# Kernel optimization log

Hardware: AMD Instinct MI355X
Metric: run time of the kernel (lower is better)

The kernel has to match this reference:

```python
import jax, jax.numpy as jnp
import numpy as np

B, N, C, H = 2, 1024, 768, 12
D = C // H
SCALE = D ** -0.5


def setup_inputs() -> dict:
    key = jax.random.key(0)
    ks = jax.random.split(key, 6)
    s = 1.0 / np.sqrt(C)
    return {
        "x": jax.random.normal(ks[0], (B, N, C), jnp.float32),
        "Wqkv": jax.random.normal(ks[1], (3 * C, C), jnp.float32) * s,   # qkv_bias=False
        "Wa": jax.random.normal(ks[2], (H, C), jnp.float32) * s,        # selective gate Linear(dim, H)
        "ba": jnp.zeros((H,), jnp.float32),
        "Wproj": jax.random.normal(ks[3], (C, C), jnp.float32) * s,
        "bproj": jnp.zeros((C,), jnp.float32),
    }


def _silu_shifted(z):
    # silu(x) + 0.5, L2-normalized over head dim (silunorm=True)
    r = jax.nn.silu(z) + 0.5
    return r / jnp.linalg.norm(r, axis=-1, keepdims=True)


def _forward(x, Wqkv, Wa, ba, Wproj, bproj):
    qkv = (x @ Wqkv.T).reshape(B, N, 3, H, D).transpose(2, 0, 3, 1, 4)  # [3,B,H,N,D]
    q = _silu_shifted(qkv[0])
    k = _silu_shifted(qkv[1])
    v = qkv[2]

    # selective forget gates: a = 1 - sigmoid(Linear(x)); torch.tensor(...) detaches -> stop_gradient
    a = jax.lax.stop_gradient(1.0 - jax.nn.sigmoid(x @ Wa.T + ba)).transpose(0, 2, 1)  # [B,H,N]
    # drop first token's gate, prepend 1 (as in the module)
    a = jnp.concatenate([jnp.ones_like(a[..., :1]), a[..., 1:]], axis=-1)

    # Causal_Mask_Selective(log(a)):
    #   A_for[i,j]  = prod_{t=j..i-1} a[t]   (j <= i)
    #   A_back[i,j] = prod_{t=i+1..j} a[t]   (j >= i)
    #   M = A_for + A_back - I
    c = jnp.cumsum(jnp.log(a), axis=-1)
    c = jnp.concatenate([jnp.zeros_like(c[..., :1]), c], axis=-1)  # [B,H,N+1], c[m] = sum log a[0..m-1]
    tri = jnp.tril(jnp.ones((N, N), bool))
    d_for = c[..., :N, None] - c[..., None, :N]      # c[i]-c[j]
    d_back = c[..., None, 1:] - c[..., 1:, None]     # c[j+1]-c[i+1]
    A_for = jnp.where(tri, jnp.exp(jnp.where(tri, d_for, 0.0)), 0.0)
    A_back = jnp.where(tri.T, jnp.exp(jnp.where(tri.T, d_back, 0.0)), 0.0)
    M = A_for + A_back - jnp.eye(N, dtype=x.dtype)

    attn = jnp.einsum('bhid,bhjd->bhij', q, k) * SCALE * M
    attn = attn / (attn.sum(axis=-1, keepdims=True) + 1e-6)  # sum-normalization, NOT softmax
    out = jnp.einsum('bhij,bhjd->bhid', attn, v).transpose(0, 2, 1, 3).reshape(B, N, C)
    return out @ Wproj.T + bproj


def reference(x, Wqkv, Wa, ba, Wproj, bproj):
    return _forward(x, Wqkv, Wa, ba, Wproj, bproj)
```

## Files before the change

kernel.cpp:

```cpp
#include <hip/hip_runtime.h>
#include <hip/hip_bf16.h>

#define BB 2
#define NN 1024
#define CC 768
#define HH 12
#define DD 64
#define SCALE_F 0.125f

typedef __attribute__((ext_vector_type(8))) __bf16 bf16x8;
typedef __attribute__((ext_vector_type(8))) unsigned short u16x8;
typedef __attribute__((ext_vector_type(4))) unsigned short u16x4;
typedef __attribute__((ext_vector_type(4))) float f32x4;

static __device__ __forceinline__ bf16x8 as_bf16x8(u16x8 v) {
  return __builtin_bit_cast(bf16x8, v);
}
static __device__ __forceinline__ unsigned short bf16u(float f) {
  __hip_bfloat16 h = __float2bfloat16(f);
  return __builtin_bit_cast(unsigned short, h);
}
static __device__ __forceinline__ void gload16(const void* g, void* l) {
  __builtin_amdgcn_global_load_lds(
      (const __attribute__((address_space(1))) unsigned int*)g,
      (__attribute__((address_space(3))) unsigned int*)l, 16, 0, 0);
}

__global__ __launch_bounds__(256) void packgate(
    const float* __restrict__ x, const float* __restrict__ Wa,
    const float* __restrict__ ba, float* __restrict__ loga,
    unsigned short* __restrict__ xb, int n0,
    const float* __restrict__ Wqkv, unsigned short* __restrict__ wqkvb, int n1,
    const float* __restrict__ Wproj, unsigned short* __restrict__ wprojb,
    int n2) {
  __shared__ float was[HH][CC];
  if (blockIdx.x < 512) {
    for (int i = threadIdx.x; i < HH * CC; i += 256)
      was[i / CC][i % CC] = Wa[i];
    __syncthreads();
    const int w = threadIdx.x >> 6, lane = threadIdx.x & 63;
    const int row = blockIdx.x * 4 + w;
    const int b = row >> 10, n = row & 1023;
    const float* xr = x + (size_t)row * CC;
    float xf[12];
#pragma unroll
    for (int j = 0; j < 12; j++) xf[j] = xr[lane + 64 * j];
    float myacc = 0.f;
#pragma unroll
    for (int h = 0; h < HH; h++) {
      float a = 0.f;
#pragma unroll
      for (int j = 0; j < 12; j++) a += xf[j] * was[h][lane + 64 * j];
#pragma unroll
      for (int off = 32; off >= 1; off >>= 1) a += __shfl_xor(a, off, 64);
      if (lane == h) myacc = a;
    }
    if (lane < HH) {
      float acc = myacc + ba[lane];
      float a = 1.f - 1.f / (1.f + __expf(-acc));
      float la = (n == 0) ? 0.f : log2f(a);
      loga[(b * HH + lane) * NN + n] = la;
    }
  } else {
    int i = (blockIdx.x - 512) * 256 + threadIdx.x;
    const float* s;
    unsigned short* d;
    if (i < n0) {
      s = x; d = xb;
    } else if (i < n0 + n1) {
      i -= n0; s = Wqkv; d = wqkvb;
    } else {
      i -= n0 + n1;
      if (i >= n2) return;
      s = Wproj; d = wprojb;
    }
    float4 v = ((const float4*)s)[i];
    u16x4 u = {bf16u(v.x), bf16u(v.y), bf16u(v.z), bf16u(v.w)};
    *(u16x4*)&d[i * 4] = u;
  }
}

template <int BM, int BN, int EPI>
__global__ __launch_bounds__(256) void gemm_mfma(
    const unsigned short* __restrict__ A, const unsigned short* __restrict__ W,
    const float* __restrict__ bias, void* __restrict__ outv,
    unsigned short* __restrict__ qp, unsigned short* __restrict__ kp,
    unsigned short* __restrict__ vtp, int M, int Nc, int K) {
  __shared__ unsigned short As[2][BM * 64];
  __shared__ unsigned short Ws[2][BN * 64];
  constexpr int FM = BM / 32, FN = BN / 32;
  const int row0 = blockIdx.y * BM;
  const int col0 = blockIdx.x * BN;
  const int t = threadIdx.x;
  const int w = t >> 6, lane = t & 63;
  const int lrow = lane & 15, lgrp = lane >> 4;
  const int wr = w >> 1, wc = w & 1;

  f32x4 acc[FM][FN] = {};

  auto STAGE = [&](int buf, int k0) {
#pragma unroll
    for (int i = 0; i < BM * 8 / 256; i++) {
      int idx = i * 256 + t;
      int row = idx >> 3, sl = (idx & 7) ^ (row & 7);
      gload16(A + (size_t)(row0 + row) * K + k0 + sl * 8, &As[buf][idx * 8]);
    }
#pragma unroll
    for (int i = 0; i < BN * 8 / 256; i++) {
      int idx = i * 256 + t;
      int row = idx >> 3, sl = (idx & 7) ^ (row & 7);
      gload16(W + (size_t)(col0 + row) * K + k0 + sl * 8, &Ws[buf][idx * 8]);
    }
  };

  const int NT = K / 64;
  STAGE(0, 0);
  __syncthreads();

  for (int tt = 0; tt < NT; tt++) {
    const int cur = tt & 1;
    if (tt + 1 < NT) STAGE(cur ^ 1, (tt + 1) * 64);

    bf16x8 af[FM][2], bf[FN][2];
#pragma unroll
    for (int m = 0; m < FM; m++) {
      int row = wr * (BM / 2) + m * 16 + lrow;
      const u16x8* p = (const u16x8*)&As[cur][row * 64];
#pragma unroll
      for (int hk = 0; hk < 2; hk++)
        af[m][hk] = as_bf16x8(p[(hk * 4 + lgrp) ^ (row & 7)]);
    }
#pragma unroll
    for (int n = 0; n < FN; n++) {
      int row = wc * (BN / 2) + n * 16 + lrow;
      const u16x8* p = (const u16x8*)&Ws[cur][row * 64];
#pragma unroll
      for (int hk = 0; hk < 2; hk++)
        bf[n][hk] = as_bf16x8(p[(hk * 4 + lgrp) ^ (row & 7)]);
    }
#pragma unroll
    for (int m = 0; m < FM; m++)
#pragma unroll
      for (int n = 0; n < FN; n++) {
        acc[m][n] = __builtin_amdgcn_mfma_f32_16x16x32_bf16(
            af[m][0], bf[n][0], acc[m][n], 0, 0, 0);
        acc[m][n] = __builtin_amdgcn_mfma_f32_16x16x32_bf16(
            af[m][1], bf[n][1], acc[m][n], 0, 0, 0);
      }
    __syncthreads();
  }

  if constexpr (EPI == 0) {
#pragma unroll
    for (int n = 0; n < FN; n++) {
      int col = col0 + wc * (BN / 2) + n * 16 + lrow;
      float bb = bias ? bias[col] : 0.f;
#pragma unroll
      for (int m = 0; m < FM; m++) {
        int rbase = row0 + wr * (BM / 2) + m * 16 + lgrp * 4;
#pragma unroll
        for (int r = 0; r < 4; r++)
          ((float*)outv)[(size_t)(rbase + r) * Nc + col] = acc[m][n][r] + bb;
      }
    }
  } else {
    const int sec = col0 / CC;
    const int h = ((col0 % CC) >> 6) + wc;
    const int rb = row0 + wr * (BM / 2);
    const int b = rb >> 10;
    const int nbase = rb & (NN - 1);
    const size_t bh = (size_t)b * HH + h;
    if (sec < 2) {
      unsigned short* dst = sec ? kp : qp;
#pragma unroll
      for (int m = 0; m < FM; m++) {
#pragma unroll
        for (int r = 0; r < 4; r++) {
          float sil[FN];
          float ss = 0.f;
#pragma unroll
          for (int n = 0; n < FN; n++) {
            float v = acc[m][n][r];
            float s = v / (1.f + __expf(-v)) + 0.5f;
            sil[n] = s;
            ss += s * s;
          }
#pragma unroll
          for (int off = 1; off <= 8; off <<= 1) ss += __shfl_xor(ss, off, 64);
          float rn = rsqrtf(ss);
          int nn = nbase + m * 16 + lgrp * 4 + r;
#pragma unroll
          for (int n = 0; n < FN; n++)
            dst[(bh * NN + nn) * DD + n * 16 + lrow] = bf16u(sil[n] * rn);
        }
      }
    } else {
#pragma unroll
      for (int m = 0; m < FM; m++) {
#pragma unroll
        for (int n = 0; n < FN; n++) {
          int d = n * 16 + lrow;
          int nn0 = nbase + m * 16 + lgrp * 4;
          u16x4 pkt = {bf16u(acc[m][n][0]), bf16u(acc[m][n][1]),
                       bf16u(acc[m][n][2]), bf16u(acc[m][n][3])};
          *(u16x4*)&vtp[(bh * DD + d) * NN + nn0] = pkt;
        }
      }
    }
  }
}

__global__ __launch_bounds__(256) void attn_mfma(
    const unsigned short* __restrict__ qp, const unsigned short* __restrict__ kp,
    const unsigned short* __restrict__ vt, const float* __restrict__ loga,
    unsigned short* __restrict__ attnout) {
  __shared__ __align__(16) unsigned char smem[45072];
  unsigned short* Ks = (unsigned short*)smem;
  unsigned short* Vs = (unsigned short*)(smem + 16384);
  unsigned short* AwB = (unsigned short*)(smem + 32768);
  float* cls = (float*)(smem + 40960);
  float* CwB = (float*)smem;
  float* RwB = (float*)(smem + 8704);

  const int qt2 = blockIdx.x & 31;
  const int bh = blockIdx.x >> 5;
  const int b = bh / HH, h = bh % HH;
  const int qrow0 = qt2 * 32;
  const int w = threadIdx.x >> 6;
  const int lane = threadIdx.x & 63;
  const int lrow = lane & 15;
  const int lgrp = lane >> 4;
  const int wq = w & 1;
  const int js = w >> 1;

  if (w == 0) {
    const float4* s4 = (const float4*)(loga + (size_t)bh * NN + lane * 16);
    float v[16];
#pragma unroll
    for (int q = 0; q < 4; q++) {
      float4 tv = s4[q];
      v[q * 4 + 0] = tv.x; v[q * 4 + 1] = tv.y;
      v[q * 4 + 2] = tv.z; v[q * 4 + 3] = tv.w;
    }
    float run = 0.f;
#pragma unroll
    for (int e = 0; e < 16; e++) { run += v[e]; v[e] = run; }
    float tot = run;
#pragma unroll
    for (int off = 1; off < 64; off <<= 1) {
      float nb = __shfl_up(tot, off, 64);
      if (lane >= off) tot += nb;
    }
    float excl = tot - run;
    if (lane == 0) cls[0] = 0.f;
#pragma unroll
    for (int e = 0; e < 16; e++) cls[1 + lane * 16 + e] = v[e] + excl;
  }

  bf16x8 qaf[2];
  {
    const u16x8* qrow_p = (const u16x8*)(qp +
        ((size_t)bh * NN + qrow0 + wq * 16 + lrow) * DD);
#pragma unroll
    for (int hk = 0; hk < 2; hk++) qaf[hk] = as_bf16x8(qrow_p[hk * 4 + lgrp]);
  }

  const int ibase = qrow0 + wq * 16 + lgrp * 4;
  float ci[4], ci1[4];
  f32x4 oacc[4] = {};
  float rs[4] = {0.f, 0.f, 0.f, 0.f};

  for (int t = 0; t < 8; t++) {
#pragma unroll
    for (int rep = 0; rep < 4; rep++) {
      int idx = rep * 256 + threadIdx.x;
      int buf = idx >> 9, row = (idx >> 3) & 63;
      int sl = (idx & 7) ^ (row & 7);
      int j0s = (buf * 8 + t) * 64;
      gload16(kp + ((size_t)bh * NN + j0s + row) * DD + sl * 8, Ks + idx * 8);
      gload16(vt + ((size_t)bh * DD + row) * NN + j0s + sl * 8, Vs + idx * 8);
    }
    __syncthreads();
    if (t == 0) {
#pragma unroll
      for (int r = 0; r < 4; r++) {
        ci[r] = cls[ibase + r];
        ci1[r] = cls[ibase + r + 1];
      }
    }

    const int j0 = (js * 8 + t) * 64;

#pragma unroll
    for (int ct = 0; ct < 4; ct++) {
      const int jl = ct * 16 + lrow;
      const int j = j0 + jl;
      f32x4 s = {};
      const u16x8* krow_p = (const u16x8*)(Ks + js * 4096 + jl * 64);
#pragma unroll
      for (int hk = 0; hk < 2; hk++) {
        bf16x8 kf = as_bf16x8(krow_p[(hk * 4 + lgrp) ^ (jl & 7)]);
        s = __builtin_amdgcn_mfma_f32_16x16x32_bf16(qaf[hk], kf, s, 0, 0, 0);
      }
      const float cj = cls[j], cj1 = cls[j + 1];
#pragma unroll
      for (int r = 0; r < 4; r++) {
        const int gi = ibase + r;
        float m = (gi > j) ? exp2f(ci[r] - cj)
                 : (gi < j) ? exp2f(cj1 - ci1[r]) : 1.0f;
        float av = s[r] * SCALE_F * m;
        rs[r] += av;
        int rowa = lgrp * 4 + r;
        AwB[w * 1024 + rowa * 64 + (jl ^ ((rowa & 7) << 3))] = bf16u(av);
      }
    }

#pragma unroll
    for (int jh = 0; jh < 2; jh++) {
      const u16x8* arow_p = (const u16x8*)(AwB + w * 1024 + lrow * 64);
      bf16x8 af = as_bf16x8(arow_p[(jh * 4 + lgrp) ^ (lrow & 7)]);
#pragma unroll
      for (int dt = 0; dt < 4; dt++) {
        const int dd = dt * 16 + lrow;
        const u16x8* vrow_p = (const u16x8*)(Vs + js * 4096 + dd * 64);
        bf16x8 vf = as_bf16x8(vrow_p[(jh * 4 + lgrp) ^ (dd & 7)]);
        oacc[dt] =
            __builtin_amdgcn_mfma_f32_16x16x32_bf16(af, vf, oacc[dt], 0, 0, 0);
      }
    }
    __syncthreads();
  }

#pragma unroll
  for (int r = 0; r < 4; r++) {
#pragma unroll
    for (int off = 1; off <= 8; off <<= 1) rs[r] += __shfl_xor(rs[r], off, 64);
  }

  if (w >= 2) {
#pragma unroll
    for (int dt = 0; dt < 4; dt++)
#pragma unroll
      for (int r = 0; r < 4; r++)
        CwB[((w - 2) * 64 + lane) * 17 + dt * 4 + r] = oacc[dt][r];
#pragma unroll
    for (int r = 0; r < 4; r++) RwB[((w - 2) * 64 + lane) * 5 + r] = rs[r];
  }
  __syncthreads();
  if (w < 2) {
#pragma unroll
    for (int r = 0; r < 4; r++) {
      rs[r] += RwB[(w * 64 + lane) * 5 + r];
      rs[r] = 1.f / (rs[r] + 1e-6f);
    }
#pragma unroll
    for (int dt = 0; dt < 4; dt++) {
#pragma unroll
      for (int r = 0; r < 4; r++) {
        const int gi = ibase + r;
        float val =
            (oacc[dt][r] + CwB[(w * 64 + lane) * 17 + dt * 4 + r]) * rs[r];
        attnout[((size_t)b * NN + gi) * CC + h * DD + dt * 16 + lrow] =
            bf16u(val);
      }
    }
  }
}

extern "C" void kernel_launch(void* const* d_in, const int* in_sizes, int n_in,
                              void* d_out, int out_size, void* d_ws,
                              size_t ws_size, hipStream_t stream) {
  const float* x = (const float*)d_in[0];
  const float* Wqkv = (const float*)d_in[1];
  const float* Wa = (const float*)d_in[2];
  const float* ba = (const float*)d_in[3];
  const float* Wproj = (const float*)d_in[4];
  const float* bproj = (const float*)d_in[5];
  float* out = (float*)d_out;

  unsigned short* obuf = (unsigned short*)d_ws;
  float* loga = (float*)(obuf + (size_t)BB * NN * CC);
  unsigned short* qp = (unsigned short*)(loga + (size_t)BB * HH * NN);
  unsigned short* kp = qp + (size_t)BB * HH * NN * DD;
  unsigned short* vt = kp + (size_t)BB * HH * NN * DD;
  unsigned short* xb = vt + (size_t)BB * HH * NN * DD;
  unsigned short* wqkvb = xb + (size_t)BB * NN * CC;
  unsigned short* wprojb = wqkvb + (size_t)3 * CC * CC;

  const int n0 = BB * NN * CC / 4, n1 = 3 * CC * CC / 4, n2 = CC * CC / 4;

  packgate<<<512 + (n0 + n1 + n2 + 255) / 256, 256, 0, stream>>>(
      x, Wa, ba, loga, xb, n0, Wqkv, wqkvb, n1, Wproj, wprojb, n2);
  {
    dim3 grid(3 * CC / 128, BB * NN / 64);
    gemm_mfma<64, 128, 2><<<grid, 256, 0, stream>>>(
        xb, wqkvb, nullptr, nullptr, qp, kp, vt, BB * NN, 3 * CC, CC);
  }
  attn_mfma<<<BB * HH * (NN / 32), 256, 0, stream>>>(qp, kp, vt, loga, obuf);
  {
    dim3 grid(CC / 64, BB * NN / 64);
    gemm_mfma<64, 64, 0><<<grid, 256, 0, stream>>>(
        obuf, wprojb, bproj, out, nullptr, nullptr, nullptr, BB * NN, CC, CC);
  }
}
```

Before: 128.7 us.

## Fuse x bf16 packing into gate pass, add MFMA priority hints, simplify mask

The gate blocks already load each x row into registers, so they now also write the bf16 copy of x. This removes the separate conversion pass and its second read of x from the pack kernel. s_setprio is raised around the MFMA sections in the GEMM and attention loops so waves issuing matrix ops get scheduling priority. The diagonal case in the mask is folded into the exp2 branch, which still gives 1 because the argument is exactly zero there. That trades a select for one extra exp2 per element on the diagonal.

```diff
diff --git a/kernel.cpp b/kernel.cpp
--- a/kernel.cpp
+++ b/kernel.cpp
@@ -29,7 +29,7 @@
 __global__ __launch_bounds__(256) void packgate(
     const float* __restrict__ x, const float* __restrict__ Wa,
     const float* __restrict__ ba, float* __restrict__ loga,
-    unsigned short* __restrict__ xb, int n0,
+    unsigned short* __restrict__ xb,
     const float* __restrict__ Wqkv, unsigned short* __restrict__ wqkvb, int n1,
     const float* __restrict__ Wproj, unsigned short* __restrict__ wprojb,
     int n2) {
@@ -45,6 +45,9 @@
     float xf[12];
 #pragma unroll
     for (int j = 0; j < 12; j++) xf[j] = xr[lane + 64 * j];
+#pragma unroll
+    for (int j = 0; j < 12; j++)
+      xb[(size_t)row * CC + lane + 64 * j] = bf16u(xf[j]);
     float myacc = 0.f;
 #pragma unroll
     for (int h = 0; h < HH; h++) {
@@ -65,12 +68,10 @@
     int i = (blockIdx.x - 512) * 256 + threadIdx.x;
     const float* s;
     unsigned short* d;
-    if (i < n0) {
-      s = x; d = xb;
-    } else if (i < n0 + n1) {
-      i -= n0; s = Wqkv; d = wqkvb;
+    if (i < n1) {
+      s = Wqkv; d = wqkvb;
     } else {
-      i -= n0 + n1;
+      i -= n1;
       if (i >= n2) return;
       s = Wproj; d = wprojb;
     }
@@ -138,6 +139,7 @@
       for (int hk = 0; hk < 2; hk++)
         bf[n][hk] = as_bf16x8(p[(hk * 4 + lgrp) ^ (row & 7)]);
     }
+    __builtin_amdgcn_s_setprio(1);
 #pragma unroll
     for (int m = 0; m < FM; m++)
 #pragma unroll
@@ -147,6 +149,7 @@
         acc[m][n] = __builtin_amdgcn_mfma_f32_16x16x32_bf16(
             af[m][1], bf[n][1], acc[m][n], 0, 0, 0);
       }
+    __builtin_amdgcn_s_setprio(0);
     __syncthreads();
   }
 
@@ -297,24 +300,26 @@
       const int j = j0 + jl;
       f32x4 s = {};
       const u16x8* krow_p = (const u16x8*)(Ks + js * 4096 + jl * 64);
+      __builtin_amdgcn_s_setprio(1);
 #pragma unroll
       for (int hk = 0; hk < 2; hk++) {
         bf16x8 kf = as_bf16x8(krow_p[(hk * 4 + lgrp) ^ (jl & 7)]);
         s = __builtin_amdgcn_mfma_f32_16x16x32_bf16(qaf[hk], kf, s, 0, 0, 0);
       }
+      __builtin_amdgcn_s_setprio(0);
       const float cj = cls[j], cj1 = cls[j + 1];
 #pragma unroll
       for (int r = 0; r < 4; r++) {
         const int gi = ibase + r;
-        float m = (gi > j) ? exp2f(ci[r] - cj)
-                 : (gi < j) ? exp2f(cj1 - ci1[r]) : 1.0f;
-        float av = s[r] * SCALE_F * m;
+        float arg = (gi > j) ? (ci[r] - cj) : (cj1 - ci1[r]);
+        float av = s[r] * SCALE_F * exp2f(arg);
         rs[r] += av;
         int rowa = lgrp * 4 + r;
         AwB[w * 1024 + rowa * 64 + (jl ^ ((rowa & 7) << 3))] = bf16u(av);
       }
     }
 
+    __builtin_amdgcn_s_setprio(1);
 #pragma unroll
     for (int jh = 0; jh < 2; jh++) {
       const u16x8* arow_p = (const u16x8*)(AwB + w * 1024 + lrow * 64);
@@ -328,6 +333,7 @@
             __builtin_amdgcn_mfma_f32_16x16x32_bf16(af, vf, oacc[dt], 0, 0, 0);
       }
     }
+    __builtin_amdgcn_s_setprio(0);
     __syncthreads();
   }
 
@@ -387,10 +393,10 @@
   unsigned short* wqkvb = xb + (size_t)BB * NN * CC;
   unsigned short* wprojb = wqkvb + (size_t)3 * CC * CC;
 
-  const int n0 = BB * NN * CC / 4, n1 = 3 * CC * CC / 4, n2 = CC * CC / 4;
-
-  packgate<<<512 + (n0 + n1 + n2 + 255) / 256, 256, 0, stream>>>(
-      x, Wa, ba, loga, xb, n0, Wqkv, wqkvb, n1, Wproj, wprojb, n2);
+  const int n1 = 3 * CC * CC / 4, n2 = CC * CC / 4;
+
+  packgate<<<512 + (n1 + n2 + 255) / 256, 256, 0, stream>>>(
+      x, Wa, ba, loga, xb, Wqkv, wqkvb, n1, Wproj, wprojb, n2);
   {
     dim3 grid(3 * CC / 128, BB * NN / 64);
     gemm_mfma<64, 128, 2><<<grid, 256, 0, stream>>>(
```

After: 128.6 us. About the same (-0.1%).
